# Kernel optimization log

Hardware: AMD Instinct MI355X
Metric: run time of the kernel (lower is better)

Reference implementation:

```python
import jax, jax.numpy as jnp
import numpy as np
import math

D_MODEL = 2048
N_HEADS = 16
HEAD_DIM = D_MODEL // N_HEADS  # 128
SEQ = 2048
BATCH = 1


def make_freqs(seq_len, head_dim, theta=10000.0):
    # standard rotary frequencies: freqs_cis = exp(i * t * inv_freq)
    inv_freq = 1.0 / (theta ** (np.arange(0, head_dim, 2, dtype=np.float32) / head_dim))
    t = np.arange(seq_len, dtype=np.float32)
    ang = np.outer(t, inv_freq)  # [seq, head_dim/2]
    return jnp.asarray(np.cos(ang)), jnp.asarray(np.sin(ang))


def setup_inputs() -> dict:
    key = jax.random.key(0)
    ks = jax.random.split(key, 6)
    x = jax.random.normal(ks[0], (BATCH, SEQ, D_MODEL), dtype=jnp.float32)
    freqs_cos, freqs_sin = make_freqs(SEQ, HEAD_DIM)
    # causal additive mask, broadcastable to [b, h, s, s]
    mask = jnp.where(jnp.tril(jnp.ones((SEQ, SEQ), dtype=bool)), 0.0, -1e9).astype(jnp.float32)[None, None]
    scale = 0.02
    wq = jax.random.normal(ks[1], (D_MODEL, D_MODEL), dtype=jnp.float32) * scale
    wk = jax.random.normal(ks[2], (D_MODEL, D_MODEL), dtype=jnp.float32) * scale
    wv = jax.random.normal(ks[3], (D_MODEL, D_MODEL), dtype=jnp.float32) * scale
    wo = jax.random.normal(ks[4], (D_MODEL, D_MODEL), dtype=jnp.float32) * scale
    return {"x": x, "freqs_cos": freqs_cos, "freqs_sin": freqs_sin, "mask": mask,
            "wq": wq, "wk": wk, "wv": wv, "wo": wo}


def _apply_rotary(q, k, cos, sin):
    # q, k: [b, s, h, hd]; cos/sin: [s, hd/2]
    def rot(t):
        tr = t.reshape(*t.shape[:-1], -1, 2)  # [b, s, h, hd/2, 2]
        re, im = tr[..., 0], tr[..., 1]
        c = cos[None, :, None, :]
        s = sin[None, :, None, :]
        # complex multiply (re + i im) * (c + i s)
        out_re = re * c - im * s
        out_im = re * s + im * c
        return jnp.stack([out_re, out_im], axis=-1).reshape(t.shape)
    return rot(q), rot(k)


def reference(x, freqs_cos, freqs_sin, mask, wq, wk, wv, wo):
    b, s, _ = x.shape
    # QKV projections (nn.Linear with no bias: x @ W^T; W is square so use x @ W
    # with W stored already-transposed -- weights here are random so x @ W is faithful math)
    q = (x @ wq).reshape(b, s, N_HEADS, HEAD_DIM)
    k = (x @ wk).reshape(b, s, N_HEADS, HEAD_DIM)
    v = (x @ wv).reshape(b, s, N_HEADS, HEAD_DIM)
    q, k = _apply_rotary(q, k, freqs_cos, freqs_sin)
    # [b, h, s_q, s_k]
    scores = jnp.einsum("bqhd,bkhd->bhqk", q, k) / math.sqrt(HEAD_DIM)
    scores = scores + mask
    probs = jax.nn.softmax(scores.astype(jnp.float32), axis=-1).astype(q.dtype)
    out = jnp.einsum("bhqk,bkhd->bqhd", probs, v).reshape(b, s, N_HEADS * HEAD_DIM)
    return out @ wo
```

## Files before the change

kernel.cpp:

```cpp
#include <hip/hip_runtime.h>
#include <hip/hip_bf16.h>
#include <math.h>

#define SEQ 2048
#define DM 2048
#define NH 16
#define HD 128
#define QKV_N 6144

typedef __bf16 bf16;
typedef __bf16 bf16x8 __attribute__((ext_vector_type(8)));
typedef __bf16 bf16x4v __attribute__((ext_vector_type(4)));
typedef __bf16 bf16x2v __attribute__((ext_vector_type(2)));
typedef float f32x4 __attribute__((ext_vector_type(4)));

__device__ inline int sw_idx32(int row, int quad) {
    return (row * 4 + (quad ^ ((row >> 1) & 3))) * 8;
}
__device__ inline int sw_idx64(int row, int chunk) {
    return (row * 8 + (chunk ^ (row & 7))) * 8;
}

__device__ inline void async16(const void* g, void* l) {
    __builtin_amdgcn_global_load_lds((const __attribute__((address_space(1))) void*)g,
                                     (__attribute__((address_space(3))) void*)l, 16, 0, 0);
}

__global__ void k_prep(const float* __restrict__ wq, const float* __restrict__ wk,
                       const float* __restrict__ wv, const float* __restrict__ wo,
                       bf16* __restrict__ wT, bf16* __restrict__ woT,
                       const float* __restrict__ x, bf16* __restrict__ xb) {
    const int z = blockIdx.z;
    int tx = threadIdx.x, ty = threadIdx.y;
    if (z == 4) {
        int bid = blockIdx.y * 64 + blockIdx.x;
        if (bid >= 1024) return;
        int i = bid * 1024 + ty * 32 + tx;
        float4 v = ((const float4*)x)[i];
        bf16x4v o;
        o.x = (bf16)v.x; o.y = (bf16)v.y; o.z = (bf16)v.z; o.w = (bf16)v.w;
        ((bf16x4v*)xb)[i] = o;
        return;
    }
    __shared__ float tile[32][33];
    const float* src = (z == 0) ? wq : (z == 1) ? wk : (z == 2) ? wv : wo;
    bf16* dst = (z < 3) ? (wT + (size_t)z * DM * DM) : woT;
    int bx = blockIdx.x * 32, by = blockIdx.y * 32;
    tile[ty][tx] = src[(size_t)(by + ty) * DM + bx + tx];
    __syncthreads();
    dst[(size_t)(bx + ty) * DM + by + tx] = (bf16)tile[tx][ty];
}

__global__ __launch_bounds__(256) void k_gemm_qkv(const bf16* __restrict__ A,
                                                  const bf16* __restrict__ Bt,
                                                  bf16* __restrict__ qkv,
                                                  bf16* __restrict__ vT,
                                                  const float* __restrict__ cosT,
                                                  const float* __restrict__ sinT) {
    const int K = DM;
    __shared__ bf16 smem[2 * 128 * 64];
    bf16* As = smem;
    bf16* Bs = smem + 128 * 64;
    const int t = threadIdx.x;
    const int lane = t & 63;
    const int w = t >> 6;
    const int wr = (w >> 1) * 64, wc = (w & 1) * 64;
    const int l15 = lane & 15, quad = lane >> 4;
    const size_t bm = (size_t)blockIdx.y * 128, bn = (size_t)blockIdx.x * 128;
    f32x4 acc[4][4];
#pragma unroll
    for (int i = 0; i < 4; ++i)
#pragma unroll
        for (int j = 0; j < 4; ++j) acc[i][j] = (f32x4){0.f, 0.f, 0.f, 0.f};

    int srow[4], sgc[4];
#pragma unroll
    for (int j = 0; j < 4; ++j) {
        int c = j * 256 + t;
        srow[j] = c >> 3;
        sgc[j] = ((c & 7) ^ (srow[j] & 7)) * 8;
    }

    for (int kt = 0; kt < K; kt += 64) {
#pragma unroll
        for (int j = 0; j < 4; ++j) {
            async16(&A[(bm + srow[j]) * K + kt + sgc[j]], &As[(j * 256 + t) * 8]);
            async16(&Bt[(bn + srow[j]) * K + kt + sgc[j]], &Bs[(j * 256 + t) * 8]);
        }
        __syncthreads();
#pragma unroll
        for (int kh = 0; kh < 2; ++kh) {
            bf16x8 af[4], bfm[4];
#pragma unroll
            for (int mi = 0; mi < 4; ++mi)
                af[mi] = *(const bf16x8*)&As[sw_idx64(wr + mi * 16 + l15, kh * 4 + quad)];
#pragma unroll
            for (int ni = 0; ni < 4; ++ni)
                bfm[ni] = *(const bf16x8*)&Bs[sw_idx64(wc + ni * 16 + l15, kh * 4 + quad)];
#pragma unroll
            for (int mi = 0; mi < 4; ++mi)
#pragma unroll
                for (int ni = 0; ni < 4; ++ni)
                    acc[mi][ni] = __builtin_amdgcn_mfma_f32_16x16x32_bf16(
                        af[mi], bfm[ni], acc[mi][ni], 0, 0, 0);
        }
        __syncthreads();
    }

    if (blockIdx.x < 32) {
        const bool is_re = (l15 & 1) == 0;
#pragma unroll
        for (int mi = 0; mi < 4; ++mi)
#pragma unroll
            for (int ni = 0; ni < 4; ++ni) {
                const int n_local = wc + ni * 16 + l15;
                const int i = n_local >> 1;
#pragma unroll
                for (int r = 0; r < 4; ++r) {
                    size_t row = bm + wr + mi * 16 + quad * 4 + r;
                    float c = cosT[row * 64 + i];
                    float sn = sinT[row * 64 + i];
                    float a = acc[mi][ni][r];
                    float p = __shfl_xor(a, 1);
                    float v = is_re ? (a * c - p * sn) : (p * sn + a * c);
                    qkv[row * QKV_N + bn + n_local] = (bf16)v;
                }
            }
    } else {
#pragma unroll
        for (int mi = 0; mi < 4; ++mi)
#pragma unroll
            for (int ni = 0; ni < 4; ++ni) {
                const int n_local = wc + ni * 16 + l15;
#pragma unroll
                for (int r = 0; r < 4; ++r) {
                    int s_local = wr + mi * 16 + quad * 4 + r;
                    smem[n_local * 128 + ((((s_local >> 3) ^ (n_local & 15)) * 8) |
                                          (s_local & 7))] = (bf16)acc[mi][ni][r];
                }
            }
        __syncthreads();
        const int n_l = t >> 1;
        const size_t ch = bn - 4096 + n_l;
#pragma unroll
        for (int j = 0; j < 8; ++j) {
            int c = (t & 1) * 8 + j;
            bf16x8 v = *(const bf16x8*)&smem[n_l * 128 + ((c ^ (n_l & 15)) * 8)];
            *(bf16x8*)&vT[ch * SEQ + bm + c * 8] = v;
        }
    }
}

template <typename OutT, int BN>
__global__ __launch_bounds__(256) void k_gemm_bt(const bf16* __restrict__ A,
                                                 const bf16* __restrict__ Bt,
                                                 OutT* __restrict__ C,
                                                 int M, int N, int K) {
    constexpr int NI = BN / 32;
    __shared__ bf16 As[128 * 64];
    __shared__ bf16 Bs[BN * 64];
    const int t = threadIdx.x;
    const int lane = t & 63;
    const int w = t >> 6;
    const int wr = (w >> 1) * 64, wc = (w & 1) * (BN / 2);
    const int l15 = lane & 15, quad = lane >> 4;
    const size_t bm = (size_t)blockIdx.y * 128, bn = (size_t)blockIdx.x * BN;
    f32x4 acc[4][NI];
#pragma unroll
    for (int i = 0; i < 4; ++i)
#pragma unroll
        for (int j = 0; j < NI; ++j) acc[i][j] = (f32x4){0.f, 0.f, 0.f, 0.f};

    for (int kt = 0; kt < K; kt += 64) {
#pragma unroll
        for (int j = 0; j < 4; ++j) {
            int c = j * 256 + t;
            int row = c >> 3, g = ((c & 7) ^ (row & 7)) * 8;
            async16(&A[(bm + row) * K + kt + g], &As[c * 8]);
        }
#pragma unroll
        for (int j = 0; j < NI; ++j) {
            int c = j * 256 + t;
            int row = c >> 3, g = ((c & 7) ^ (row & 7)) * 8;
            async16(&Bt[(bn + row) * K + kt + g], &Bs[c * 8]);
        }
        __syncthreads();
#pragma unroll
        for (int kh = 0; kh < 2; ++kh) {
            bf16x8 af[4], bfm[NI];
#pragma unroll
            for (int mi = 0; mi < 4; ++mi)
                af[mi] = *(const bf16x8*)&As[sw_idx64(wr + mi * 16 + l15, kh * 4 + quad)];
#pragma unroll
            for (int ni = 0; ni < NI; ++ni)
                bfm[ni] = *(const bf16x8*)&Bs[sw_idx64(wc + ni * 16 + l15, kh * 4 + quad)];
#pragma unroll
            for (int mi = 0; mi < 4; ++mi)
#pragma unroll
                for (int ni = 0; ni < NI; ++ni)
                    acc[mi][ni] = __builtin_amdgcn_mfma_f32_16x16x32_bf16(
                        af[mi], bfm[ni], acc[mi][ni], 0, 0, 0);
        }
        __syncthreads();
    }
#pragma unroll
    for (int mi = 0; mi < 4; ++mi)
#pragma unroll
        for (int ni = 0; ni < NI; ++ni)
#pragma unroll
            for (int r = 0; r < 4; ++r) {
                size_t row = bm + wr + mi * 16 + quad * 4 + r;
                size_t col = bn + wc + ni * 16 + l15;
                C[row * (size_t)N + col] = (OutT)acc[mi][ni][r];
            }
}

__global__ __launch_bounds__(256) void k_flash(const bf16* __restrict__ qkv,
                                               const bf16* __restrict__ vT,
                                               bf16* __restrict__ out) {
    __shared__ bf16 Ks[4][64 * 32];
    __shared__ bf16 Vs[2][128 * 32];
    __shared__ bf16 Pl[4][16][72];
    const int t = threadIdx.x;
    const int lane = t & 63;
    const int w = t >> 6;
    const int l15 = lane & 15, quad = lane >> 4;
    const int b = blockIdx.x;
    const int h = (b & 7) * 2 + ((b >> 3) & 1);
    const int qb = 31 - (b >> 4);
    const int q0w = qb * 64 + w * 16;
    const float sc = 0.08838834764831845f;

    const size_t qrow = (size_t)(q0w + l15) * QKV_N + h * HD;
    bf16x8 aq[4];
#pragma unroll
    for (int u = 0; u < 4; ++u)
        aq[u] = *(const bf16x8*)&qkv[qrow + u * 32 + quad * 8];

    f32x4 o[8];
#pragma unroll
    for (int c = 0; c < 8; ++c) o[c] = (f32x4){0.f, 0.f, 0.f, 0.f};
    float l_r[4] = {0.f, 0.f, 0.f, 0.f};

    const int srow = t >> 2;
    const int ch = ((t & 3) ^ ((t >> 3) & 3)) * 8;

    for (int kt = 0; kt <= qb; ++kt) {
        const int kbase = kt * 64;
#pragma unroll
        for (int u = 0; u < 4; ++u)
            async16(&qkv[(size_t)(kbase + srow) * QKV_N + DM + h * HD + u * 32 + ch],
                    &Ks[u][t * 8]);
#pragma unroll
        for (int j = 0; j < 2; ++j) {
            async16(&vT[(size_t)(h * HD + srow) * SEQ + kbase + j * 32 + ch],
                    &Vs[j][t * 8]);
            async16(&vT[(size_t)(h * HD + 64 + srow) * SEQ + kbase + j * 32 + ch],
                    &Vs[j][(t + 256) * 8]);
        }
        __syncthreads();
        f32x4 s[4];
#pragma unroll
        for (int sub = 0; sub < 4; ++sub) {
            f32x4 z = (f32x4){0.f, 0.f, 0.f, 0.f};
#pragma unroll
            for (int u = 0; u < 4; ++u) {
                bf16x8 kb = *(const bf16x8*)&Ks[u][sw_idx32(sub * 16 + l15, quad)];
                z = __builtin_amdgcn_mfma_f32_16x16x32_bf16(aq[u], kb, z, 0, 0, 0);
            }
            s[sub] = z;
        }
        const bool masked = (kt == qb);
#pragma unroll
        for (int sub = 0; sub < 4; ++sub)
#pragma unroll
            for (int r = 0; r < 4; ++r) {
                float p = __expf(s[sub][r] * sc);
                if (masked)
                    p = (kbase + sub * 16 + l15 <= q0w + quad * 4 + r) ? p : 0.f;
                l_r[r] += p;
                Pl[w][quad * 4 + r][sub * 16 + l15] = (bf16)p;
            }
        __syncthreads();
        bf16x8 pf0 = *(const bf16x8*)&Pl[w][l15][quad * 8];
        bf16x8 pf1 = *(const bf16x8*)&Pl[w][l15][32 + quad * 8];
#pragma unroll
        for (int c = 0; c < 8; ++c) {
            bf16x8 vb0 = *(const bf16x8*)&Vs[0][sw_idx32(c * 16 + l15, quad)];
            o[c] = __builtin_amdgcn_mfma_f32_16x16x32_bf16(pf0, vb0, o[c], 0, 0, 0);
            bf16x8 vb1 = *(const bf16x8*)&Vs[1][sw_idx32(c * 16 + l15, quad)];
            o[c] = __builtin_amdgcn_mfma_f32_16x16x32_bf16(pf1, vb1, o[c], 0, 0, 0);
        }
        __syncthreads();
    }

    float rl[4];
#pragma unroll
    for (int r = 0; r < 4; ++r) {
        float l = l_r[r];
        l += __shfl_xor(l, 1, 16);
        l += __shfl_xor(l, 2, 16);
        l += __shfl_xor(l, 4, 16);
        l += __shfl_xor(l, 8, 16);
        rl[r] = 1.0f / l;
    }
#pragma unroll
    for (int c = 0; c < 8; ++c)
#pragma unroll
        for (int r = 0; r < 4; ++r)
            out[(size_t)(q0w + quad * 4 + r) * DM + h * HD + c * 16 + l15] =
                (bf16)(o[c][r] * rl[r]);
}

extern "C" void kernel_launch(void* const* d_in, const int* in_sizes, int n_in,
                              void* d_out, int out_size, void* d_ws, size_t ws_size,
                              hipStream_t stream) {
    const float* x  = (const float*)d_in[0];
    const float* fc = (const float*)d_in[1];
    const float* fs = (const float*)d_in[2];
    const float* wq = (const float*)d_in[4];
    const float* wk = (const float*)d_in[5];
    const float* wv = (const float*)d_in[6];
    const float* wo = (const float*)d_in[7];
    float* out = (float*)d_out;

    char* ws = (char*)d_ws;
    bf16* xb  = (bf16*)(ws);
    bf16* wT  = (bf16*)(ws + (size_t)(8u  << 20));
    bf16* woT = (bf16*)(ws + (size_t)(32u << 20));
    bf16* qkv = (bf16*)(ws + (size_t)(40u << 20));
    bf16* vT  = (bf16*)(ws + (size_t)(64u << 20));

    k_prep<<<dim3(64, 64, 5), dim3(32, 32), 0, stream>>>(wq, wk, wv, wo, wT, woT, x, xb);
    k_gemm_qkv<<<dim3(48, 16), 256, 0, stream>>>(xb, wT, qkv, vT, fc, fs);
    k_flash<<<512, 256, 0, stream>>>(qkv, vT, xb);
    k_gemm_bt<float, 64><<<dim3(32, 16), 256, 0, stream>>>(xb, woT, out, SEQ, DM, DM);
}
```

Measured before the change: 327.7 us.

## Permute Q/K weight columns and stage packed bf16 cos/sin in LDS for rotary epilogue

The Q/K weight transpose now permutes output columns so each lane's accumulator tiles hold the real and imaginary parts of a rotary pair side by side. This removes the cross-lane shuffle and lets each lane write a packed bf16 pair. Cos and sin are converted once into an interleaved bf16 table, and each GEMM block loads its rows into swizzled LDS with async copies instead of reading scattered fp32 values from global memory. The cost is an extra prep pass and a bf16 rounding of cos/sin, which lowers precision slightly.

New measurement: 327.5 us. About the same (-0.1%).

```diff
diff --git a/kernel.cpp b/kernel.cpp
--- a/kernel.cpp
+++ b/kernel.cpp
@@ -29,7 +29,9 @@
 __global__ void k_prep(const float* __restrict__ wq, const float* __restrict__ wk,
                        const float* __restrict__ wv, const float* __restrict__ wo,
                        bf16* __restrict__ wT, bf16* __restrict__ woT,
-                       const float* __restrict__ x, bf16* __restrict__ xb) {
+                       const float* __restrict__ x, bf16* __restrict__ xb,
+                       const float* __restrict__ fc, const float* __restrict__ fs,
+                       bf16* __restrict__ csT) {
     const int z = blockIdx.z;
     int tx = threadIdx.x, ty = threadIdx.y;
     if (z == 4) {
@@ -42,21 +44,35 @@
         ((bf16x4v*)xb)[i] = o;
         return;
     }
+    if (z == 5) {
+        int bid = blockIdx.y * 64 + blockIdx.x;
+        if (bid >= 128) return;
+        int idx = bid * 1024 + ty * 32 + tx;
+        bf16x2v cs;
+        cs.x = (bf16)fc[idx];
+        cs.y = (bf16)fs[idx];
+        ((bf16x2v*)csT)[idx] = cs;
+        return;
+    }
     __shared__ float tile[32][33];
     const float* src = (z == 0) ? wq : (z == 1) ? wk : (z == 2) ? wv : wo;
     bf16* dst = (z < 3) ? (wT + (size_t)z * DM * DM) : woT;
     int bx = blockIdx.x * 32, by = blockIdx.y * 32;
     tile[ty][tx] = src[(size_t)(by + ty) * DM + bx + tx];
     __syncthreads();
-    dst[(size_t)(bx + ty) * DM + by + tx] = (bf16)tile[tx][ty];
+    int n = bx + ty;
+    if (z < 2) {
+        int nh = n & 127;
+        n = (n & ~127) | (((nh >> 5) << 5) + ((nh & 1) << 4) + ((nh & 31) >> 1));
+    }
+    dst[(size_t)n * DM + by + tx] = (bf16)tile[tx][ty];
 }
 
 __global__ __launch_bounds__(256) void k_gemm_qkv(const bf16* __restrict__ A,
                                                   const bf16* __restrict__ Bt,
                                                   bf16* __restrict__ qkv,
                                                   bf16* __restrict__ vT,
-                                                  const float* __restrict__ cosT,
-                                                  const float* __restrict__ sinT) {
+                                                  const bf16* __restrict__ csT) {
     const int K = DM;
     __shared__ bf16 smem[2 * 128 * 64];
     bf16* As = smem;
@@ -108,22 +124,34 @@
     }
 
     if (blockIdx.x < 32) {
-        const bool is_re = (l15 & 1) == 0;
+#pragma unroll
+        for (int j = 0; j < 8; ++j) {
+            int c = j * 256 + t;
+            int row = c >> 4;
+            int g16 = ((c & 15) ^ (row & 15)) * 8;
+            async16(&csT[(bm + row) * 128 + g16], &smem[c * 8]);
+        }
+        __syncthreads();
+        const bf16x2v* cs32 = (const bf16x2v*)smem;
 #pragma unroll
         for (int mi = 0; mi < 4; ++mi)
 #pragma unroll
-            for (int ni = 0; ni < 4; ++ni) {
-                const int n_local = wc + ni * 16 + l15;
-                const int i = n_local >> 1;
-#pragma unroll
-                for (int r = 0; r < 4; ++r) {
-                    size_t row = bm + wr + mi * 16 + quad * 4 + r;
-                    float c = cosT[row * 64 + i];
-                    float sn = sinT[row * 64 + i];
-                    float a = acc[mi][ni][r];
-                    float p = __shfl_xor(a, 1);
-                    float v = is_re ? (a * c - p * sn) : (p * sn + a * c);
-                    qkv[row * QKV_N + bn + n_local] = (bf16)v;
+            for (int r = 0; r < 4; ++r) {
+                const int row_l = wr + mi * 16 + quad * 4 + r;
+                const int rk = row_l & 15;
+#pragma unroll
+                for (int g = 0; g < 2; ++g) {
+                    const int base_i = ((wc + 32 * g) & 127) >> 1;
+                    const int word_i = base_i + l15;
+                    const int slot = (word_i >> 2) ^ rk;
+                    bf16x2v cs = cs32[(row_l * 16 + slot) * 4 + (word_i & 3)];
+                    float c = (float)cs.x, sn = (float)cs.y;
+                    float re = acc[mi][2 * g][r];
+                    float im = acc[mi][2 * g + 1][r];
+                    bf16x2v o;
+                    o.x = (bf16)(re * c - im * sn);
+                    o.y = (bf16)(re * sn + im * c);
+                    *(bf16x2v*)&qkv[(bm + row_l) * QKV_N + bn + wc + 32 * g + 2 * l15] = o;
                 }
             }
     } else {
@@ -330,9 +358,11 @@
     bf16* woT = (bf16*)(ws + (size_t)(32u << 20));
     bf16* qkv = (bf16*)(ws + (size_t)(40u << 20));
     bf16* vT  = (bf16*)(ws + (size_t)(64u << 20));
-
-    k_prep<<<dim3(64, 64, 5), dim3(32, 32), 0, stream>>>(wq, wk, wv, wo, wT, woT, x, xb);
-    k_gemm_qkv<<<dim3(48, 16), 256, 0, stream>>>(xb, wT, qkv, vT, fc, fs);
+    bf16* csT = (bf16*)(ws + (size_t)(72u << 20));
+
+    k_prep<<<dim3(64, 64, 6), dim3(32, 32), 0, stream>>>(wq, wk, wv, wo, wT, woT,
+                                                         x, xb, fc, fs, csT);
+    k_gemm_qkv<<<dim3(48, 16), 256, 0, stream>>>(xb, wT, qkv, vT, csT);
     k_flash<<<512, 256, 0, stream>>>(qkv, vT, xb);
     k_gemm_bt<float, 64><<<dim3(32, 16), 256, 0, stream>>>(xb, woT, out, SEQ, DM, DM);
 }
```
